# Kernel optimization log

Hardware: AMD Instinct MI355X
Metric: run time of the kernel (lower is better)

The kernel has to match this reference:

```python
import jax, jax.numpy as jnp
import numpy as np

B, S, D = 2, 2048, 1024
H = 16
HD = D // H  # 64


def setup_inputs() -> dict:
    key = jax.random.key(0)
    ks = jax.random.split(key, 9)
    s = 1.0 / np.sqrt(D)
    x = jax.random.normal(ks[0], (B, S, D), dtype=jnp.float32)
    Wq = jax.random.normal(ks[1], (D, D), dtype=jnp.float32) * s
    Wk = jax.random.normal(ks[2], (D, D), dtype=jnp.float32) * s
    Wv = jax.random.normal(ks[3], (D, D), dtype=jnp.float32) * s
    Wo = jax.random.normal(ks[4], (D, D), dtype=jnp.float32) * s
    bq = jnp.zeros((D,), jnp.float32)
    bk = jnp.zeros((D,), jnp.float32)
    bv = jnp.zeros((D,), jnp.float32)
    bo = jnp.zeros((D,), jnp.float32)
    # causal mask, broadcastable to (B, H, S, S)
    mask = jnp.tril(jnp.ones((S, S), dtype=bool))[None, None, :, :]
    return {"x": x, "Wq": Wq, "bq": bq, "Wk": Wk, "bk": bk,
            "Wv": Wv, "bv": bv, "Wo": Wo, "bo": bo, "mask": mask}


def _split_heads(t):
    # (B, S, D) -> (B, H, S, HD)
    b, s, _ = t.shape
    return t.reshape(b, s, H, HD).transpose(0, 2, 1, 3)


def reference(x, Wq, bq, Wk, bk, Wv, bv, Wo, bo, mask):
    q = _split_heads(x @ Wq + bq)
    k = _split_heads(x @ Wk + bk)
    v = _split_heads(x @ Wv + bv)
    scale = 1.0 / jnp.sqrt(jnp.asarray(HD, dtype=q.dtype))
    scores = jnp.einsum('bhqd,bhkd->bhqk', q, k) * scale
    large_neg = jnp.finfo(scores.dtype).min
    scores = jnp.where(mask, scores, large_neg)
    attn = jax.nn.softmax(scores, axis=-1)
    out = jnp.einsum('bhqk,bhkd->bhqd', attn, v)  # (B,H,S,HD)
    out = out.transpose(0, 2, 1, 3).reshape(x.shape[0], x.shape[1], D)
    return out @ Wo + bo
```

## Files before the change

kernel.cpp:

```cpp
#include <hip/hip_runtime.h>
#include <hip/hip_bf16.h>

typedef __attribute__((ext_vector_type(8))) short bf16x8;
typedef __attribute__((ext_vector_type(4))) float f32x4;

#define B_DIM  2
#define S_DIM  2048
#define D_DIM  1024
#define H_DIM  16
#define HD_DIM 64

__device__ __forceinline__ float bf2f(ushort u) {
    union { unsigned int ui; float f; } c; c.ui = ((unsigned int)u) << 16; return c.f;
}
__device__ __forceinline__ ushort f2bf(float f) {
    __hip_bfloat16 h = __float2bfloat16(f);
    return *reinterpret_cast<ushort*>(&h);
}

__global__ __launch_bounds__(256) void detect_kernel(const ushort* __restrict__ x,
                                                     int* __restrict__ flag) {
    __shared__ int any;
    int tid = threadIdx.x;
    if (tid == 0) any = 0;
    __syncthreads();
    int cnt = 0;
    for (int j = 0; j < 64; ++j) {
        ushort u = x[tid * 64 + j];
        if (((u >> 7) & 0xFF) == 0xFF) cnt++;
    }
    if (cnt) atomicOr(&any, 1);
    __syncthreads();
    if (tid == 0) *flag = any ? 1 : 0;
}

__global__ __launch_bounds__(256) void convx_kernel(const void* __restrict__ src,
                                                    ushort* __restrict__ dst,
                                                    const int* __restrict__ flag, int n8) {
    int i = blockIdx.x * 256 + threadIdx.x;
    if (i >= n8) return;
    if (*flag) {
        const float* s = (const float*)src;
        f32x4 a = *(const f32x4*)&s[(size_t)i * 8];
        f32x4 b = *(const f32x4*)&s[(size_t)i * 8 + 4];
        bf16x8 o;
        o[0] = f2bf(a.x); o[1] = f2bf(a.y); o[2] = f2bf(a.z); o[3] = f2bf(a.w);
        o[4] = f2bf(b.x); o[5] = f2bf(b.y); o[6] = f2bf(b.z); o[7] = f2bf(b.w);
        *(bf16x8*)&dst[(size_t)i * 8] = o;
    } else {
        *(bf16x8*)&dst[(size_t)i * 8] = *(const bf16x8*)&((const ushort*)src)[(size_t)i * 8];
    }
}

__global__ __launch_bounds__(256) void convb_kernel(const void* b0, const void* b1,
                                                    const void* b2, const void* b3,
                                                    float* __restrict__ dst,
                                                    const int* __restrict__ flag) {
    int i = blockIdx.x * 256 + threadIdx.x;
    int w = i >> 10, j = i & 1023;
    const void* s = (w == 0) ? b0 : (w == 1) ? b1 : (w == 2) ? b2 : b3;
    dst[i] = (*flag) ? ((const float*)s)[j] : bf2f(((const ushort*)s)[j]);
}

__global__ __launch_bounds__(256) void transpose_w_kernel(const void* __restrict__ Wq,
                                                          const void* __restrict__ Wk,
                                                          const void* __restrict__ Wv,
                                                          const void* __restrict__ Wo,
                                                          ushort* __restrict__ Wqkvt,
                                                          ushort* __restrict__ Wot,
                                                          const int* __restrict__ flag) {
    __shared__ ushort tile[64][72];
    int tid = threadIdx.x;
    int z = blockIdx.z;
    const void* src = (z == 0) ? Wq : (z == 1) ? Wk : (z == 2) ? Wv : Wo;
    ushort* dst = (z < 3) ? (Wqkvt + (size_t)z * D_DIM * D_DIM) : Wot;
    int r0 = blockIdx.y * 64, c0 = blockIdx.x * 64;
    bool isf32 = (*flag != 0);
#pragma unroll
    for (int p = 0; p < 2; ++p) {
        int r = p * 32 + (tid >> 3);
        int c = (tid & 7) * 8;
        if (isf32) {
            const float* s = (const float*)src;
            f32x4 a = *(const f32x4*)&s[(size_t)(r0 + r) * D_DIM + c0 + c];
            f32x4 b = *(const f32x4*)&s[(size_t)(r0 + r) * D_DIM + c0 + c + 4];
            tile[r][c + 0] = f2bf(a.x); tile[r][c + 1] = f2bf(a.y);
            tile[r][c + 2] = f2bf(a.z); tile[r][c + 3] = f2bf(a.w);
            tile[r][c + 4] = f2bf(b.x); tile[r][c + 5] = f2bf(b.y);
            tile[r][c + 6] = f2bf(b.z); tile[r][c + 7] = f2bf(b.w);
        } else {
            *(bf16x8*)&tile[r][c] =
                *(const bf16x8*)&((const ushort*)src)[(size_t)(r0 + r) * D_DIM + c0 + c];
        }
    }
    __syncthreads();
#pragma unroll
    for (int p = 0; p < 2; ++p) {
        int n  = p * 32 + (tid >> 3);
        int cc = (tid & 7) * 8;
        bf16x8 v;
#pragma unroll
        for (int e = 0; e < 8; ++e) v[e] = (short)tile[cc + e][n];
        *(bf16x8*)&dst[(size_t)(c0 + n) * D_DIM + r0 + cc] = v;
    }
}

__global__ __launch_bounds__(256) void transpose_v_kernel(const ushort* __restrict__ src,
                                                          ushort* __restrict__ dst) {
    __shared__ ushort tile[64][72];
    int tid = threadIdx.x;
    int s0 = blockIdx.x * 64;
    int bh = blockIdx.y;
    const ushort* sb = src + (size_t)bh * S_DIM * HD_DIM;
    ushort* db = dst + (size_t)bh * HD_DIM * S_DIM;
#pragma unroll
    for (int p = 0; p < 2; ++p) {
        int r = p * 32 + (tid >> 3);
        int c = (tid & 7) * 8;
        *(bf16x8*)&tile[r][c] = *(const bf16x8*)&sb[(size_t)(s0 + r) * HD_DIM + c];
    }
    __syncthreads();
#pragma unroll
    for (int p = 0; p < 2; ++p) {
        int n  = p * 32 + (tid >> 3);
        int cc = (tid & 7) * 8;
        bf16x8 v;
#pragma unroll
        for (int e = 0; e < 8; ++e) v[e] = (short)tile[cc + e][n];
        *(bf16x8*)&db[(size_t)n * S_DIM + s0 + cc] = v;
    }
}

#define G2 72
__global__ __launch_bounds__(256) void gemm128_kernel(const ushort* __restrict__ A,
                                                      const ushort* __restrict__ Bt,
                                                      const float* __restrict__ bias,
                                                      void* __restrict__ out,
                                                      const int* __restrict__ flag,
                                                      int mode) {
    __shared__ ushort As[128 * G2];
    __shared__ ushort Bs[128 * G2];
    int tid  = threadIdx.x;
    int wave = tid >> 6;
    int lane = tid & 63;
    int l16  = lane & 15;
    int quad = lane >> 4;
    int m0   = blockIdx.y * 128;
    int n0   = blockIdx.x * 128;
    int wm   = wave >> 1;
    int wn   = wave & 1;
    const int K = 1024;

    f32x4 acc[4][4];
#pragma unroll
    for (int i = 0; i < 4; ++i)
#pragma unroll
        for (int j = 0; j < 4; ++j) acc[i][j] = (f32x4){0.f, 0.f, 0.f, 0.f};

    int srow = tid >> 3;
    int scol = (tid & 7) * 8;

    bf16x8 ar[4], br[4];
#pragma unroll
    for (int p = 0; p < 4; ++p) {
        ar[p] = *(const bf16x8*)&A[(size_t)(m0 + srow + 32 * p) * K + scol];
        br[p] = *(const bf16x8*)&Bt[(size_t)(n0 + srow + 32 * p) * K + scol];
    }

    for (int kt = 0; kt < 16; ++kt) {
        __syncthreads();
#pragma unroll
        for (int p = 0; p < 4; ++p) {
            *(bf16x8*)&As[(srow + 32 * p) * G2 + scol] = ar[p];
            *(bf16x8*)&Bs[(srow + 32 * p) * G2 + scol] = br[p];
        }
        __syncthreads();
        if (kt < 15) {
            int k0 = (kt + 1) * 64;
#pragma unroll
            for (int p = 0; p < 4; ++p) {
                ar[p] = *(const bf16x8*)&A[(size_t)(m0 + srow + 32 * p) * K + k0 + scol];
                br[p] = *(const bf16x8*)&Bt[(size_t)(n0 + srow + 32 * p) * K + k0 + scol];
            }
        }
#pragma unroll
        for (int kb = 0; kb < 64; kb += 32) {
            bf16x8 af[4], bf[4];
#pragma unroll
            for (int i = 0; i < 4; ++i)
                af[i] = *(const bf16x8*)&As[(wm * 64 + i * 16 + l16) * G2 + kb + quad * 8];
#pragma unroll
            for (int j = 0; j < 4; ++j)
                bf[j] = *(const bf16x8*)&Bs[(wn * 64 + j * 16 + l16) * G2 + kb + quad * 8];
#pragma unroll
            for (int i = 0; i < 4; ++i)
#pragma unroll
                for (int j = 0; j < 4; ++j)
                    acc[i][j] = __builtin_amdgcn_mfma_f32_16x16x32_bf16(af[i], bf[j],
                                                                        acc[i][j], 0, 0, 0);
        }
    }

    int outf32 = (mode == 1) ? *flag : 0;
    const size_t TSZ = (size_t)B_DIM * H_DIM * S_DIM * HD_DIM;
#pragma unroll
    for (int j = 0; j < 4; ++j) {
        int n = n0 + wn * 64 + j * 16 + l16;
        float bv = bias[n];
#pragma unroll
        for (int i = 0; i < 4; ++i)
#pragma unroll
            for (int r = 0; r < 4; ++r) {
                int m = m0 + wm * 64 + i * 16 + quad * 4 + r;
                float v = acc[i][j][r] + bv;
                if (mode == 0) {
                    int which = n >> 10;
                    int n1 = n & 1023;
                    int h = n1 >> 6, hd = n1 & 63;
                    int b = m >> 11, s = m & (S_DIM - 1);
                    if (which == 0) v *= 0.125f;
                    ((ushort*)out)[which * TSZ +
                        ((((size_t)(b * H_DIM + h)) * S_DIM + s) << 6) + hd] = f2bf(v);
                } else if (outf32) {
                    ((float*)out)[(size_t)m * D_DIM + n] = v;
                } else {
                    ((ushort*)out)[(size_t)m * D_DIM + n] = f2bf(v);
                }
            }
    }
}

#define SLD 72
__global__ __launch_bounds__(256) void attn_kernel(const ushort* __restrict__ Qg,
                                                   const ushort* __restrict__ Kg,
                                                   const ushort* __restrict__ Vt,
                                                   ushort* __restrict__ attn_out) {
    __shared__ ushort Ks[64 * SLD];
    __shared__ ushort Vs[64 * SLD];
    __shared__ ushort Ss[64 * SLD];
    int tid  = threadIdx.x;
    int wave = tid >> 6;
    int lane = tid & 63;
    int l16  = lane & 15;
    int quad = lane >> 4;
    int bh   = blockIdx.x;
    int qt   = (int)gridDim.y - 1 - (int)blockIdx.y;
    int q0   = qt * 64;

    const ushort* Qb = Qg + (size_t)bh * S_DIM * HD_DIM;
    const ushort* Kb = Kg + (size_t)bh * S_DIM * HD_DIM;
    const ushort* Vb = Vt + (size_t)bh * HD_DIM * S_DIM;

    int qrow = q0 + wave * 16 + l16;
    bf16x8 qf[2];
#pragma unroll
    for (int ks = 0; ks < 2; ++ks)
        qf[ks] = *(const bf16x8*)&Qb[(size_t)qrow * HD_DIM + ks * 32 + quad * 8];

    f32x4 o[4];
#pragma unroll
    for (int i = 0; i < 4; ++i) o[i] = (f32x4){0.f, 0.f, 0.f, 0.f};
    float rsum[4] = {0.f, 0.f, 0.f, 0.f};

    int srow = tid >> 3;
    int scol = (tid & 7) * 8;

    bf16x8 kr[2], vr[2];
#pragma unroll
    for (int p = 0; p < 2; ++p) {
        kr[p] = *(const bf16x8*)&Kb[(size_t)(srow + 32 * p) * HD_DIM + scol];
        vr[p] = *(const bf16x8*)&Vb[(size_t)(srow + 32 * p) * S_DIM + scol];
    }

    int ntiles = qt + 1;
    for (int t = 0; t < ntiles; ++t) {
        __syncthreads();
#pragma unroll
        for (int p = 0; p < 2; ++p) {
            *(bf16x8*)&Ks[(srow + 32 * p) * SLD + scol] = kr[p];
            *(bf16x8*)&Vs[(srow + 32 * p) * SLD + scol] = vr[p];
        }
        __syncthreads();
        if (t < qt) {
            int k1 = (t + 1) * 64;
#pragma unroll
            for (int p = 0; p < 2; ++p) {
                kr[p] = *(const bf16x8*)&Kb[(size_t)(k1 + srow + 32 * p) * HD_DIM + scol];
                vr[p] = *(const bf16x8*)&Vb[(size_t)(srow + 32 * p) * S_DIM + k1 + scol];
            }
        }

        f32x4 sc[4];
#pragma unroll
        for (int i = 0; i < 4; ++i) sc[i] = (f32x4){0.f, 0.f, 0.f, 0.f};
#pragma unroll
        for (int ks = 0; ks < 2; ++ks)
#pragma unroll
            for (int nb = 0; nb < 4; ++nb) {
                bf16x8 kf = *(const bf16x8*)&Ks[(nb * 16 + l16) * SLD + ks * 32 + quad * 8];
                sc[nb] = __builtin_amdgcn_mfma_f32_16x16x32_bf16(qf[ks], kf, sc[nb], 0, 0, 0);
            }

        if (t == qt) {
            int k0 = t * 64;
            int qglob = q0 + wave * 16 + quad * 4;
#pragma unroll
            for (int nb = 0; nb < 4; ++nb) {
                int key = k0 + nb * 16 + l16;
#pragma unroll
                for (int r = 0; r < 4; ++r)
                    if (key > qglob + r) sc[nb][r] = -1e30f;
            }
        }

#pragma unroll
        for (int nb = 0; nb < 4; ++nb)
#pragma unroll
            for (int r = 0; r < 4; ++r) {
                float p = __expf(sc[nb][r]);
                rsum[r] += p;
                Ss[(wave * 16 + quad * 4 + r) * SLD + nb * 16 + l16] = f2bf(p);
            }

        bf16x8 pf[2];
#pragma unroll
        for (int ks = 0; ks < 2; ++ks)
            pf[ks] = *(const bf16x8*)&Ss[(wave * 16 + l16) * SLD + ks * 32 + quad * 8];

#pragma unroll
        for (int ks = 0; ks < 2; ++ks)
#pragma unroll
            for (int nb = 0; nb < 4; ++nb) {
                bf16x8 vf = *(const bf16x8*)&Vs[(nb * 16 + l16) * SLD + ks * 32 + quad * 8];
                o[nb] = __builtin_amdgcn_mfma_f32_16x16x32_bf16(pf[ks], vf, o[nb], 0, 0, 0);
            }
    }

#pragma unroll
    for (int d = 1; d < 16; d <<= 1)
#pragma unroll
        for (int r = 0; r < 4; ++r)
            rsum[r] += __shfl_xor(rsum[r], d, 64);

    int b = bh >> 4, h = bh & 15;
    float inv[4];
#pragma unroll
    for (int r = 0; r < 4; ++r) inv[r] = 1.f / rsum[r];
#pragma unroll
    for (int nb = 0; nb < 4; ++nb)
#pragma unroll
        for (int r = 0; r < 4; ++r) {
            int q = q0 + wave * 16 + quad * 4 + r;
            attn_out[(size_t)(b * S_DIM + q) * D_DIM + h * HD_DIM + nb * 16 + l16] =
                f2bf(o[nb][r] * inv[r]);
        }
}

extern "C" void kernel_launch(void* const* d_in, const int* in_sizes, int n_in,
                              void* d_out, int out_size, void* d_ws, size_t ws_size,
                              hipStream_t stream) {
    const void* x  = d_in[0];
    const void* Wq = d_in[1];
    const void* bq = d_in[2];
    const void* Wk = d_in[3];
    const void* bk = d_in[4];
    const void* Wv = d_in[5];
    const void* bv = d_in[6];
    const void* Wo = d_in[7];
    const void* bo = d_in[8];

    char* ws = (char*)d_ws;
    const size_t MB = 1024 * 1024;
    const size_t base = 64 * 1024;
    int*    flag   = (int*)ws;
    float*  biasf  = (float*)(ws + 4096);
    ushort* xc     = (ushort*)(ws + base);
    ushort* Wqkvt  = (ushort*)(ws + base + 8  * MB);
    ushort* Wot    = (ushort*)(ws + base + 14 * MB);
    ushort* Qc     = (ushort*)(ws + base + 16 * MB);
    ushort* Vc     = (ushort*)(ws + base + 32 * MB);
    ushort* Vtp    = (ushort*)(ws + base + 40 * MB);
    ushort* attn   = xc;

    dim3 tb(256);

    detect_kernel<<<1, tb, 0, stream>>>((const ushort*)x, flag);

    int n8 = (B_DIM * S_DIM * D_DIM) / 8;
    convx_kernel<<<n8 / 256, tb, 0, stream>>>(x, xc, flag, n8);
    convb_kernel<<<16, tb, 0, stream>>>(bq, bk, bv, bo, biasf, flag);

    dim3 tw(D_DIM / 64, D_DIM / 64, 4);
    transpose_w_kernel<<<tw, tb, 0, stream>>>(Wq, Wk, Wv, Wo, Wqkvt, Wot, flag);

    dim3 gq(3 * D_DIM / 128, (B_DIM * S_DIM) / 128);
    gemm128_kernel<<<gq, tb, 0, stream>>>(xc, Wqkvt, biasf, Qc, flag, 0);

    dim3 vg(S_DIM / 64, B_DIM * H_DIM);
    transpose_v_kernel<<<vg, tb, 0, stream>>>(Vc, Vtp);

    dim3 ag(B_DIM * H_DIM, S_DIM / 64);
    attn_kernel<<<ag, tb, 0, stream>>>(Qc, Qc + (size_t)B_DIM * H_DIM * S_DIM * HD_DIM,
                                       Vtp, attn);

    dim3 go(D_DIM / 128, (B_DIM * S_DIM) / 128);
    gemm128_kernel<<<go, tb, 0, stream>>>(attn, Wot, biasf + 3072, d_out, flag, 1);
}
```

Baseline: 227.9 us.

## Load GEMM tiles directly into LDS with XOR-swizzled layout

Replaces the register-staged global-to-LDS copy in the 128x128 GEMM with direct global_load_lds 16-byte transfers, dropping the padded layout for an XOR-swizzled one that avoids LDS bank conflicts. This removes the register round-trip and the explicit LDS stores. It also drops the software prefetch of the next K tile, so global loads no longer overlap with the MFMA work of the previous tile. The added trailing barrier keeps the single LDS buffer from being overwritten while it is still being read.

```diff
diff --git a/kernel.cpp b/kernel.cpp
--- a/kernel.cpp
+++ b/kernel.cpp
@@ -16,6 +16,12 @@
 __device__ __forceinline__ ushort f2bf(float f) {
     __hip_bfloat16 h = __float2bfloat16(f);
     return *reinterpret_cast<ushort*>(&h);
+}
+
+__device__ __forceinline__ void async_cp16(const ushort* g, ushort* l) {
+    __builtin_amdgcn_global_load_lds(
+        (const __attribute__((address_space(1))) void*)g,
+        (__attribute__((address_space(3))) void*)l, 16, 0, 0);
 }
 
 __global__ __launch_bounds__(256) void detect_kernel(const ushort* __restrict__ x,
@@ -131,15 +137,14 @@
     }
 }
 
-#define G2 72
 __global__ __launch_bounds__(256) void gemm128_kernel(const ushort* __restrict__ A,
                                                       const ushort* __restrict__ Bt,
                                                       const float* __restrict__ bias,
                                                       void* __restrict__ out,
                                                       const int* __restrict__ flag,
                                                       int mode) {
-    __shared__ ushort As[128 * G2];
-    __shared__ ushort Bs[128 * G2];
+    __shared__ ushort As[128 * 64];
+    __shared__ ushort Bs[128 * 64];
     int tid  = threadIdx.x;
     int wave = tid >> 6;
     int lane = tid & 63;
@@ -157,41 +162,32 @@
 #pragma unroll
         for (int j = 0; j < 4; ++j) acc[i][j] = (f32x4){0.f, 0.f, 0.f, 0.f};
 
-    int srow = tid >> 3;
-    int scol = (tid & 7) * 8;
-
-    bf16x8 ar[4], br[4];
-#pragma unroll
-    for (int p = 0; p < 4; ++p) {
-        ar[p] = *(const bf16x8*)&A[(size_t)(m0 + srow + 32 * p) * K + scol];
-        br[p] = *(const bf16x8*)&Bt[(size_t)(n0 + srow + 32 * p) * K + scol];
-    }
+    int lrow = lane >> 3;
+    int gcol = ((lane & 7) ^ lrow) * 8;
+    int sw   = l16 & 7;
 
     for (int kt = 0; kt < 16; ++kt) {
+        int k0 = kt * 64;
+#pragma unroll
+        for (int j = 0; j < 4; ++j) {
+            int chunk = wave * 4 + j;
+            int grow  = chunk * 8 + lrow;
+            async_cp16(&A[(size_t)(m0 + grow) * K + k0 + gcol], &As[chunk * 512]);
+            async_cp16(&Bt[(size_t)(n0 + grow) * K + k0 + gcol], &Bs[chunk * 512]);
+        }
         __syncthreads();
-#pragma unroll
-        for (int p = 0; p < 4; ++p) {
-            *(bf16x8*)&As[(srow + 32 * p) * G2 + scol] = ar[p];
-            *(bf16x8*)&Bs[(srow + 32 * p) * G2 + scol] = br[p];
-        }
-        __syncthreads();
-        if (kt < 15) {
-            int k0 = (kt + 1) * 64;
-#pragma unroll
-            for (int p = 0; p < 4; ++p) {
-                ar[p] = *(const bf16x8*)&A[(size_t)(m0 + srow + 32 * p) * K + k0 + scol];
-                br[p] = *(const bf16x8*)&Bt[(size_t)(n0 + srow + 32 * p) * K + k0 + scol];
-            }
-        }
-#pragma unroll
-        for (int kb = 0; kb < 64; kb += 32) {
+
+#pragma unroll
+        for (int kb = 0; kb < 2; ++kb) {
             bf16x8 af[4], bf[4];
 #pragma unroll
             for (int i = 0; i < 4; ++i)
-                af[i] = *(const bf16x8*)&As[(wm * 64 + i * 16 + l16) * G2 + kb + quad * 8];
+                af[i] = *(const bf16x8*)&As[(wm * 64 + i * 16 + l16) * 64 +
+                                            (((kb * 4 + quad) ^ sw) << 3)];
 #pragma unroll
             for (int j = 0; j < 4; ++j)
-                bf[j] = *(const bf16x8*)&Bs[(wn * 64 + j * 16 + l16) * G2 + kb + quad * 8];
+                bf[j] = *(const bf16x8*)&Bs[(wn * 64 + j * 16 + l16) * 64 +
+                                            (((kb * 4 + quad) ^ sw) << 3)];
 #pragma unroll
             for (int i = 0; i < 4; ++i)
 #pragma unroll
@@ -199,6 +195,7 @@
                     acc[i][j] = __builtin_amdgcn_mfma_f32_16x16x32_bf16(af[i], bf[j],
                                                                         acc[i][j], 0, 0, 0);
         }
+        __syncthreads();
     }
 
     int outf32 = (mode == 1) ? *flag : 0;
```

New measurement: 227.4 us. Within noise of the previous version (-0.2%).
